# Performance work log

Measured on AMD Instinct MI355X. Metric: run time of the kernel, lower is better.

The kernel has to match this reference:

```python
import jax, jax.numpy as jnp
import numpy as np

NEG_SLOPE = 0.2  # PyG GATConv default leaky_relu slope
EPS = 1e-16     # PyG softmax denominator epsilon


def gat_conv(x, src, dst, W, att_src, att_dst, bias, concat, num_nodes):
    """PyG-style GATConv (eval mode, dropout disabled).
    x: [N, F_in]; W: [F_in, H*C]; att_src/att_dst: [H, C]; bias: [H*C] or [C].
    Messages flow src -> dst; softmax is per destination node."""
    H, C = att_src.shape
    h = (x @ W).reshape(num_nodes, H, C)                      # [N,H,C]
    a_src = jnp.sum(h * att_src[None], axis=-1)               # [N,H]
    a_dst = jnp.sum(h * att_dst[None], axis=-1)               # [N,H]
    e = jax.nn.leaky_relu(a_src[src] + a_dst[dst], NEG_SLOPE) # [E,H]
    # numerically-stable segment softmax over edges grouped by dst
    m = jax.ops.segment_max(e, dst, num_segments=num_nodes)   # [N,H]
    ex = jnp.exp(e - m[dst])                                  # [E,H]
    s = jax.ops.segment_sum(ex, dst, num_segments=num_nodes)  # [N,H]
    alpha = ex / (s[dst] + EPS)                               # [E,H]
    msg = h[src] * alpha[..., None]                           # [E,H,C]
    out = jax.ops.segment_sum(msg, dst, num_segments=num_nodes)  # [N,H,C]
    if concat:
        out = out.reshape(num_nodes, H * C)
    else:
        out = out.mean(axis=1)                                # [N,C]
    return out + bias, alpha


def setup_inputs() -> dict:
    key = jax.random.key(0)
    ks = jax.random.split(key, 20)
    N, E = 50000, 500000
    F_node = 128       # num_node_features
    SED = 128          # sentence_embedding_dim
    HID = 64           # hidden_channels
    H = 2              # num_heads

    def g(k, shape, scale=0.05):
        return jax.random.normal(k, shape, dtype=jnp.float32) * scale

    return {
        "x": jax.random.normal(ks[0], (N, SED), dtype=jnp.float32),
        "edge_index": jax.random.randint(ks[1], (2, E), 0, N, dtype=jnp.int64),
        "cls_emb": jax.random.normal(ks[2], (768,), dtype=jnp.float32),
        # fc0: Linear(768, SED)
        "fc0_w": g(ks[3], (SED, 768)), "fc0_b": g(ks[4], (SED,)),
        # conv1: GATConv(2*SED -> HID, heads=H, concat=True)
        "W1": g(ks[5], (2 * SED, H * HID)),
        "att_src1": g(ks[6], (H, HID)), "att_dst1": g(ks[7], (H, HID)),
        "bias1": g(ks[8], (H * HID,)),
        # conv2: GATConv(H*HID -> F_node, heads=H, concat=False)
        "W2": g(ks[9], (H * HID, H * F_node)),
        "att_src2": g(ks[10], (H, F_node)), "att_dst2": g(ks[11], (H, F_node)),
        "bias2": g(ks[12], (F_node,)),
        # edge MLP head
        "fc2_w": g(ks[13], (F_node, 2 * F_node)), "fc2_b": g(ks[14], (F_node,)),
        "fc3_w": g(ks[15], (1, F_node)), "fc3_b": g(ks[16], (1,)),
    }


def reference(x, edge_index, cls_emb, fc0_w, fc0_b,
              W1, att_src1, att_dst1, bias1,
              W2, att_src2, att_dst2, bias2,
              fc2_w, fc2_b, fc3_w, fc3_b):
    N = x.shape[0]
    src, dst = edge_index[0], edge_index[1]
    # sentence embedding projection + broadcast-concat to every node
    sent = fc0_w @ cls_emb + fc0_b                                # [SED]
    h = jnp.concatenate([x, jnp.broadcast_to(sent, (N, sent.shape[0]))], axis=1)
    h, _ = gat_conv(h, src, dst, W1, att_src1, att_dst1, bias1, True, N)
    h = jax.nn.elu(h)
    h, _ = gat_conv(h, src, dst, W2, att_src2, att_dst2, bias2, False, N)
    # edge head: gather endpoints, concat, MLP, sigmoid
    edge_input = jnp.concatenate([h[src], h[dst]], axis=1)        # [E, 2*F]
    z = jax.nn.relu(edge_input @ fc2_w.T + fc2_b)                 # [E, F]
    logits = z @ fc3_w.T + fc3_b                                  # [E, 1]
    return jax.nn.sigmoid(logits)
```

## Files before the change

kernel.cpp:

```cpp
#include <hip/hip_runtime.h>
#include <hip/hip_bf16.h>
#include <math.h>


typedef short short8 __attribute__((ext_vector_type(8)));
typedef float floatx4 __attribute__((ext_vector_type(4)));
typedef float v2f __attribute__((ext_vector_type(2)));
typedef unsigned uint2v __attribute__((ext_vector_type(2)));

__device__ __forceinline__ float wave_allreduce_sum(float v) {
    #pragma unroll
    for (int off = 1; off < 64; off <<= 1) v += __shfl_xor(v, off, 64);
    return v;
}
__device__ __forceinline__ v2f bfpair(unsigned v) {
    uint2v t; t.x = v << 16; t.y = v & 0xFFFF0000u;
    return __builtin_bit_cast(v2f, t);
}
__device__ __forceinline__ unsigned short bfbits(float f) {
    return __builtin_bit_cast(unsigned short, __float2bfloat16(f));
}
__device__ __forceinline__ unsigned packbf(float a, float b) {
    return ((unsigned)bfbits(b) << 16) | (unsigned)bfbits(a);
}
__device__ __forceinline__ float lrelu(float v) { return v > 0.f ? v : 0.2f * v; }

__global__ void prep_kernel(const float* __restrict__ cls, const float* __restrict__ fc0_w,
                            const float* __restrict__ fc0_b, const float* __restrict__ W1,
                            const float* __restrict__ W2, const float* __restrict__ fc2_w,
                            float* __restrict__ c1,
                            __hip_bfloat16* __restrict__ w1frag,
                            __hip_bfloat16* __restrict__ w2frag,
                            __hip_bfloat16* __restrict__ fc2frag) {
    int tid = threadIdx.x;
    if (blockIdx.x == 0) {
        __shared__ float s_sent[128];
        if (tid < 128) {
            float acc = fc0_b[tid];
            const float* row = fc0_w + (size_t)tid * 768;
            for (int k = 0; k < 768; ++k) acc += row[k] * cls[k];
            s_sent[tid] = acc;
        }
        __syncthreads();
        if (tid < 128) {
            float acc = 0.f;
            for (int k = 0; k < 128; ++k) acc += s_sent[k] * W1[(128 + k) * 128 + tid];
            c1[tid] = acc;
        }
    }
    int gstride = gridDim.x * blockDim.x;
    int g = blockIdx.x * blockDim.x + tid;
    for (int i = g; i < 16384; i += gstride) {
        int j = i & 7, l = (i >> 3) & 63, nt = (i >> 9) & 7, kt = (i >> 12) & 3;
        int k = kt * 32 + (l >> 4) * 8 + j;
        int n = nt * 16 + (l & 15);
        w1frag[i] = __float2bfloat16(W1[k * 128 + n]);
    }
    for (int i = g; i < 32768; i += gstride) {
        int j = i & 7, l = (i >> 3) & 63, nt = (i >> 9) & 15, kt = (i >> 13) & 3;
        int k = kt * 32 + (l >> 4) * 8 + j;
        int n = nt * 16 + (l & 15);
        w2frag[i] = __float2bfloat16(W2[k * 256 + n]);
    }
    for (int i = g; i < 32768; i += gstride) {
        int j = i & 7, l = (i >> 3) & 63, nt = (i >> 9) & 15, kt = (i >> 13) & 3;
        int k = kt * 32 + (l >> 4) * 8 + j;
        int n = nt * 16 + (l & 15);
        float v = (n < 128) ? fc2_w[n * 256 + k] : fc2_w[(n - 128) * 256 + 128 + k];
        fc2frag[i] = __float2bfloat16(v);
    }
}

__global__ void count_kernel(const int* __restrict__ dst, int* __restrict__ counts, int E) {
    int e = blockIdx.x * blockDim.x + threadIdx.x;
    if (e < E) atomicAdd(&counts[dst[e]], 1);
}

__global__ void __launch_bounds__(256) bsum_kernel(const int* __restrict__ counts,
                                                   int* __restrict__ bsum, int N) {
    int base = blockIdx.x * 1024;
    int tid = threadIdx.x;
    int v = 0;
    #pragma unroll
    for (int k = 0; k < 4; ++k) {
        int idx = base + k * 256 + tid;
        if (idx < N) v += counts[idx];
    }
    #pragma unroll
    for (int off = 1; off < 64; off <<= 1) v += __shfl_xor(v, off, 64);
    __shared__ int ws[4];
    if ((tid & 63) == 0) ws[tid >> 6] = v;
    __syncthreads();
    if (tid == 0) bsum[blockIdx.x] = ws[0] + ws[1] + ws[2] + ws[3];
}

__global__ void top_scan_kernel(const int* __restrict__ bsum, int* __restrict__ boff, int nb) {
    int lane = threadIdx.x;
    int v = (lane < nb) ? bsum[lane] : 0;
    int x = v;
    #pragma unroll
    for (int off = 1; off < 64; off <<= 1) {
        int t = __shfl_up(x, off, 64);
        if (lane >= off) x += t;
    }
    if (lane < nb) boff[lane] = x - v;
}

__global__ void __launch_bounds__(1024) local_scan_kernel(const int* __restrict__ counts,
                                                          const int* __restrict__ boff,
                                                          int* __restrict__ row, int* __restrict__ woff,
                                                          int N, int E) {
    int tid = threadIdx.x, lane = tid & 63, wv = tid >> 6;
    int base = blockIdx.x * 1024;
    __shared__ int wsum[16];
    int v = (base + tid < N) ? counts[base + tid] : 0;
    int x = v;
    #pragma unroll
    for (int off = 1; off < 64; off <<= 1) {
        int t = __shfl_up(x, off, 64);
        if (lane >= off) x += t;
    }
    if (lane == 63) wsum[wv] = x;
    __syncthreads();
    if (wv == 0 && lane < 16) {
        int y = wsum[lane];
        #pragma unroll
        for (int off = 1; off < 16; off <<= 1) {
            int t = __shfl_up(y, off, 64);
            if (lane >= off) y += t;
        }
        wsum[lane] = y;
    }
    __syncthreads();
    int excl = boff[blockIdx.x] + (wv ? wsum[wv - 1] : 0) + x - v;
    if (base + tid < N) { row[base + tid] = excl; woff[base + tid] = excl; }
    if (blockIdx.x == 0 && tid == 0) row[N] = E;
}

__global__ void scatter_kernel(const int* __restrict__ src, const int* __restrict__ dst,
                               int* __restrict__ woff, int* __restrict__ srcs, int E) {
    int e = blockIdx.x * blockDim.x + threadIdx.x;
    if (e < E) {
        int pos = atomicAdd(&woff[dst[e]], 1);
        srcs[pos] = src[e];
    }
}

__global__ void __launch_bounds__(256) gemm1_mfma_kernel(
        const float* __restrict__ x, const __hip_bfloat16* __restrict__ wfrag,
        const float* __restrict__ c1, const float* __restrict__ att_s, const float* __restrict__ att_d,
        __hip_bfloat16* __restrict__ h1bf, float* __restrict__ a_src, float* __restrict__ a_dst, int N) {
    int lane = threadIdx.x & 63, wv = threadIdx.x >> 6;
    int lo = lane & 15, quad = lane >> 4;
    int rowbase = (blockIdx.x * 4 + wv) * 16;
    if (rowbase >= N) return;
    int arow = rowbase + lo; if (arow >= N) arow = N - 1;
    const float* ap = x + (size_t)arow * 128 + quad * 8;
    floatx4 acc[8];
    #pragma unroll
    for (int nt = 0; nt < 8; ++nt) acc[nt] = (floatx4){0.f, 0.f, 0.f, 0.f};
    const short8* bf = (const short8*)wfrag;
    #pragma unroll
    for (int kt = 0; kt < 4; ++kt) {
        float4 fa = *(const float4*)(ap + kt * 32);
        float4 fb = *(const float4*)(ap + kt * 32 + 4);
        short8 a;
        a[0] = (short)bfbits(fa.x); a[1] = (short)bfbits(fa.y);
        a[2] = (short)bfbits(fa.z); a[3] = (short)bfbits(fa.w);
        a[4] = (short)bfbits(fb.x); a[5] = (short)bfbits(fb.y);
        a[6] = (short)bfbits(fb.z); a[7] = (short)bfbits(fb.w);
        #pragma unroll
        for (int nt = 0; nt < 8; ++nt)
            acc[nt] = __builtin_amdgcn_mfma_f32_16x16x32_bf16(a, bf[(kt * 8 + nt) * 64 + lane], acc[nt], 0, 0, 0);
    }
    float ps0[4] = {0,0,0,0}, ps1[4] = {0,0,0,0}, pd0[4] = {0,0,0,0}, pd1[4] = {0,0,0,0};
    #pragma unroll
    for (int nt = 0; nt < 8; ++nt) {
        int ch = nt * 16 + lo;
        float cv = c1[ch], as_v = att_s[ch], ad_v = att_d[ch];
        #pragma unroll
        for (int r = 0; r < 4; ++r) {
            int row = rowbase + quad * 4 + r;
            float val = acc[nt][r] + cv;
            if (row < N) ((unsigned short*)h1bf)[(size_t)row * 128 + ch] = bfbits(val);
            if (nt < 4) { ps0[r] += val * as_v; pd0[r] += val * ad_v; }
            else        { ps1[r] += val * as_v; pd1[r] += val * ad_v; }
        }
    }
    #pragma unroll
    for (int r = 0; r < 4; ++r) {
        int row = rowbase + quad * 4 + r;
        float v0 = ps0[r], v1 = ps1[r], v2 = pd0[r], v3 = pd1[r];
        #pragma unroll
        for (int off = 1; off < 16; off <<= 1) {
            v0 += __shfl_xor(v0, off, 64); v1 += __shfl_xor(v1, off, 64);
            v2 += __shfl_xor(v2, off, 64); v3 += __shfl_xor(v3, off, 64);
        }
        if (lo == 0 && row < N) {
            a_src[row * 2 + 0] = v0; a_src[row * 2 + 1] = v1;
            a_dst[row * 2 + 0] = v2; a_dst[row * 2 + 1] = v3;
        }
    }
}

__global__ void __launch_bounds__(256) agg1_csr_kernel(
        const int* __restrict__ row, const int* __restrict__ srcs,
        const float* __restrict__ a_src, const float* __restrict__ a_dst,
        const unsigned* __restrict__ h1u, const float* __restrict__ bias1,
        unsigned* __restrict__ hmid_u, int N) {
    int d = blockIdx.x * 4 + (threadIdx.x >> 6);
    if (d >= N) return;
    int lane = threadIdx.x & 63;
    int beg = row[d], end = row[d + 1];
    int g = lane >> 4, q = lane & 15;
    float2 adp = ((const float2*)a_dst)[d];
    float den0 = 0.f, den1 = 0.f;
    v2f facc2[4];
    #pragma unroll
    for (int m = 0; m < 4; ++m) facc2[m] = (v2f){0.f, 0.f};
    for (int b = beg; b < end; b += 64) {
        int i = b + lane;
        int s = 0; float e0 = 0.f, e1 = 0.f;
        if (i < end) {
            s = srcs[i];
            float2 as = ((const float2*)a_src)[s];
            e0 = __expf(lrelu(as.x + adp.x));
            e1 = __expf(lrelu(as.y + adp.y));
            den0 += e0; den1 += e1;
        }
        int cnt = min(64, end - b);
        int rounds = (cnt + 3) >> 2;
        float w0 = __shfl(e0, g, 64);
        float w1 = __shfl(e1, g, 64);
        int   sj = __shfl(s,  g, 64);
        float wgt = (q < 8) ? w0 : w1;
        uint4 u = ((const uint4*)(h1u + (size_t)sj * 64))[q];
        for (int j = 0; j < rounds; ++j) {
            int sl2 = 4 * j + 4 + g; sl2 = sl2 > 63 ? 63 : sl2;
            float w0n = __shfl(e0, sl2, 64);
            float w1n = __shfl(e1, sl2, 64);
            int   sjn = __shfl(s,  sl2, 64);
            uint4 un = ((const uint4*)(h1u + (size_t)sjn * 64))[q];
            float wgtn = (q < 8) ? w0n : w1n;
            facc2[0] += bfpair(u.x) * wgt;
            facc2[1] += bfpair(u.y) * wgt;
            facc2[2] += bfpair(u.z) * wgt;
            facc2[3] += bfpair(u.w) * wgt;
            u = un; wgt = wgtn;
        }
    }
    den0 = wave_allreduce_sum(den0);
    den1 = wave_allreduce_sum(den1);
    #pragma unroll
    for (int m = 0; m < 4; ++m) {
        facc2[m].x += __shfl_xor(facc2[m].x, 16, 64);
        facc2[m].y += __shfl_xor(facc2[m].y, 16, 64);
        facc2[m].x += __shfl_xor(facc2[m].x, 32, 64);
        facc2[m].y += __shfl_xor(facc2[m].y, 32, 64);
    }
    if (lane < 16) {
        float inv = (lane < 8) ? 1.f / (den0 + 1e-16f) : 1.f / (den1 + 1e-16f);
        int c0 = 8 * lane;
        float v[8];
        #pragma unroll
        for (int m = 0; m < 4; ++m) {
            float va = facc2[m].x * inv + bias1[c0 + 2 * m];
            float vb = facc2[m].y * inv + bias1[c0 + 2 * m + 1];
            v[2 * m]     = va > 0.f ? va : expm1f(va);
            v[2 * m + 1] = vb > 0.f ? vb : expm1f(vb);
        }
        uint4 o;
        o.x = packbf(v[0], v[1]); o.y = packbf(v[2], v[3]);
        o.z = packbf(v[4], v[5]); o.w = packbf(v[6], v[7]);
        ((uint4*)(hmid_u + (size_t)d * 64))[lane] = o;
    }
}

__global__ void __launch_bounds__(256) gemm2_mfma_kernel(
        const __hip_bfloat16* __restrict__ hmid, const __hip_bfloat16* __restrict__ wfrag,
        const float* __restrict__ att_s, const float* __restrict__ att_d,
        __hip_bfloat16* __restrict__ h2pre, float* __restrict__ a_src, float* __restrict__ a_dst, int N) {
    int lane = threadIdx.x & 63, wv = threadIdx.x >> 6;
    int lo = lane & 15, quad = lane >> 4;
    int rowbase = (blockIdx.x * 4 + wv) * 16;
    if (rowbase >= N) return;
    int arow = rowbase + lo; if (arow >= N) arow = N - 1;
    const __hip_bfloat16* ap = hmid + (size_t)arow * 128 + quad * 8;
    floatx4 acc[16];
    #pragma unroll
    for (int nt = 0; nt < 16; ++nt) acc[nt] = (floatx4){0.f, 0.f, 0.f, 0.f};
    const short8* bf = (const short8*)wfrag;
    #pragma unroll
    for (int kt = 0; kt < 4; ++kt) {
        short8 a = *(const short8*)(ap + kt * 32);
        #pragma unroll
        for (int nt = 0; nt < 16; ++nt)
            acc[nt] = __builtin_amdgcn_mfma_f32_16x16x32_bf16(a, bf[(kt * 16 + nt) * 64 + lane], acc[nt], 0, 0, 0);
    }
    float ps0[4] = {0,0,0,0}, ps1[4] = {0,0,0,0}, pd0[4] = {0,0,0,0}, pd1[4] = {0,0,0,0};
    #pragma unroll
    for (int nt = 0; nt < 16; ++nt) {
        int ch = nt * 16 + lo;
        float as_v = att_s[ch], ad_v = att_d[ch];
        #pragma unroll
        for (int r = 0; r < 4; ++r) {
            int row = rowbase + quad * 4 + r;
            float val = acc[nt][r];
            if (row < N) ((unsigned short*)h2pre)[(size_t)row * 256 + ch] = bfbits(val);
            if (nt < 8) { ps0[r] += val * as_v; pd0[r] += val * ad_v; }
            else        { ps1[r] += val * as_v; pd1[r] += val * ad_v; }
        }
    }
    #pragma unroll
    for (int r = 0; r < 4; ++r) {
        int row = rowbase + quad * 4 + r;
        float v0 = ps0[r], v1 = ps1[r], v2 = pd0[r], v3 = pd1[r];
        #pragma unroll
        for (int off = 1; off < 16; off <<= 1) {
            v0 += __shfl_xor(v0, off, 64); v1 += __shfl_xor(v1, off, 64);
            v2 += __shfl_xor(v2, off, 64); v3 += __shfl_xor(v3, off, 64);
        }
        if (lo == 0 && row < N) {
            a_src[row * 2 + 0] = v0; a_src[row * 2 + 1] = v1;
            a_dst[row * 2 + 0] = v2; a_dst[row * 2 + 1] = v3;
        }
    }
}

__global__ void __launch_bounds__(256) agg2_csr_kernel(
        const int* __restrict__ row, const int* __restrict__ srcs,
        const float* __restrict__ a_src, const float* __restrict__ a_dst,
        const unsigned* __restrict__ h2u, const float* __restrict__ bias2,
        unsigned* __restrict__ h2bf_u, int N) {
    int d = blockIdx.x * 4 + (threadIdx.x >> 6);
    if (d >= N) return;
    int lane = threadIdx.x & 63;
    int beg = row[d], end = row[d + 1];
    int g = lane >> 5, q = lane & 31;
    float2 adp = ((const float2*)a_dst)[d];
    float den0 = 0.f, den1 = 0.f;
    v2f facc2[4];
    #pragma unroll
    for (int m = 0; m < 4; ++m) facc2[m] = (v2f){0.f, 0.f};
    for (int b = beg; b < end; b += 64) {
        int i = b + lane;
        int s = 0; float e0 = 0.f, e1 = 0.f;
        if (i < end) {
            s = srcs[i];
            float2 as = ((const float2*)a_src)[s];
            e0 = __expf(lrelu(as.x + adp.x));
            e1 = __expf(lrelu(as.y + adp.y));
            den0 += e0; den1 += e1;
        }
        int cnt = min(64, end - b);
        int rounds = (cnt + 1) >> 1;
        float w0 = __shfl(e0, g, 64);
        float w1 = __shfl(e1, g, 64);
        int   sj = __shfl(s,  g, 64);
        float wgt = (q < 16) ? w0 : w1;
        uint4 u = ((const uint4*)(h2u + (size_t)sj * 128))[q];
        for (int j = 0; j < rounds; ++j) {
            int sl2 = 2 * j + 2 + g; sl2 = sl2 > 63 ? 63 : sl2;
            float w0n = __shfl(e0, sl2, 64);
            float w1n = __shfl(e1, sl2, 64);
            int   sjn = __shfl(s,  sl2, 64);
            uint4 un = ((const uint4*)(h2u + (size_t)sjn * 128))[q];
            float wgtn = (q < 16) ? w0n : w1n;
            facc2[0] += bfpair(u.x) * wgt;
            facc2[1] += bfpair(u.y) * wgt;
            facc2[2] += bfpair(u.z) * wgt;
            facc2[3] += bfpair(u.w) * wgt;
            u = un; wgt = wgtn;
        }
    }
    den0 = wave_allreduce_sum(den0);
    den1 = wave_allreduce_sum(den1);
    float inv = (q < 16) ? 0.5f / (den0 + 1e-16f) : 0.5f / (den1 + 1e-16f);
    #pragma unroll
    for (int m = 0; m < 4; ++m) {
        facc2[m].x += __shfl_xor(facc2[m].x, 32, 64);
        facc2[m].y += __shfl_xor(facc2[m].y, 32, 64);
        facc2[m] *= inv;
        facc2[m].x += __shfl_xor(facc2[m].x, 16, 64);
        facc2[m].y += __shfl_xor(facc2[m].y, 16, 64);
    }
    if (lane < 16) {
        int c0 = 8 * lane;
        uint4 o;
        o.x = packbf(facc2[0].x + bias2[c0 + 0], facc2[0].y + bias2[c0 + 1]);
        o.y = packbf(facc2[1].x + bias2[c0 + 2], facc2[1].y + bias2[c0 + 3]);
        o.z = packbf(facc2[2].x + bias2[c0 + 4], facc2[2].y + bias2[c0 + 5]);
        o.w = packbf(facc2[3].x + bias2[c0 + 6], facc2[3].y + bias2[c0 + 7]);
        ((uint4*)(h2bf_u + (size_t)d * 64))[lane] = o;
    }
}

__global__ void __launch_bounds__(256) zsd_mfma_kernel(
        const __hip_bfloat16* __restrict__ h2bf, const __hip_bfloat16* __restrict__ wfrag,
        const float* __restrict__ fc2_b, __hip_bfloat16* __restrict__ zsd, int N) {
    int lane = threadIdx.x & 63, wv = threadIdx.x >> 6;
    int lo = lane & 15, quad = lane >> 4;
    int rowbase = (blockIdx.x * 4 + wv) * 16;
    if (rowbase >= N) return;
    int arow = rowbase + lo; if (arow >= N) arow = N - 1;
    const __hip_bfloat16* ap = h2bf + (size_t)arow * 128 + quad * 8;
    floatx4 acc[16];
    #pragma unroll
    for (int nt = 0; nt < 16; ++nt) acc[nt] = (floatx4){0.f, 0.f, 0.f, 0.f};
    const short8* bf = (const short8*)wfrag;
    #pragma unroll
    for (int kt = 0; kt < 4; ++kt) {
        short8 a = *(const short8*)(ap + kt * 32);
        #pragma unroll
        for (int nt = 0; nt < 16; ++nt)
            acc[nt] = __builtin_amdgcn_mfma_f32_16x16x32_bf16(a, bf[(kt * 16 + nt) * 64 + lane], acc[nt], 0, 0, 0);
    }
    #pragma unroll
    for (int nt = 0; nt < 16; ++nt) {
        int ch = nt * 16 + lo;
        float bv = (nt >= 8) ? fc2_b[ch - 128] : 0.f;
        #pragma unroll
        for (int r = 0; r < 4; ++r) {
            int row = rowbase + quad * 4 + r;
            if (row < N) ((unsigned short*)zsd)[(size_t)row * 256 + ch] = bfbits(acc[nt][r] + bv);
        }
    }
}

__global__ void __launch_bounds__(256) edge_zsd_kernel(
        const int* __restrict__ src, const int* __restrict__ dst,
        const unsigned* __restrict__ zsd_u, const float* __restrict__ fc3_w,
        const float* __restrict__ fc3_b, float* __restrict__ out, int E) {
    int lane = threadIdx.x & 63, wv = threadIdx.x >> 6;
    int g = lane >> 5, r = (lane >> 4) & 1, q = lane & 15;
    int base = (blockIdx.x * 4 + wv) * 16;
    if (base >= E) return;
    v2f f30 = {fc3_w[8 * q + 4 * r + 0], fc3_w[8 * q + 4 * r + 1]};
    v2f f31 = {fc3_w[8 * q + 4 * r + 2], fc3_w[8 * q + 4 * r + 3]};
    float b3 = fc3_b[0];
    #pragma unroll
    for (int j = 0; j < 8; ++j) {
        int e = base + 2 * j + g;
        int ec = e < E ? e : E - 1;
        int node = r ? dst[ec] : src[ec];
        uint4 mine = ((const uint4*)(zsd_u + (size_t)node * 128 + (r << 6)))[q];
        unsigned sx = (unsigned)__shfl_xor((int)mine.x, 16, 64);
        unsigned sy = (unsigned)__shfl_xor((int)mine.y, 16, 64);
        unsigned sz = (unsigned)__shfl_xor((int)mine.z, 16, 64);
        unsigned sw = (unsigned)__shfl_xor((int)mine.w, 16, 64);
        unsigned mA = r ? mine.z : mine.x;
        unsigned mB = r ? mine.w : mine.y;
        unsigned oA = r ? sz : sx;
        unsigned oB = r ? sw : sy;
        v2f sA = bfpair(mA) + bfpair(oA);
        v2f sB = bfpair(mB) + bfpair(oB);
        sA.x = fmaxf(sA.x, 0.f); sA.y = fmaxf(sA.y, 0.f);
        sB.x = fmaxf(sB.x, 0.f); sB.y = fmaxf(sB.y, 0.f);
        v2f p2 = sA * f30 + sB * f31;
        float p = p2.x + p2.y;
        #pragma unroll
        for (int off = 1; off < 32; off <<= 1) p += __shfl_xor(p, off, 64);
        if ((lane & 31) == 0 && e < E)
            out[e] = 1.f / (1.f + expf(-(p + b3)));
    }
}

extern "C" void kernel_launch(void* const* d_in, const int* in_sizes, int n_in,
                              void* d_out, int out_size, void* d_ws, size_t ws_size,
                              hipStream_t stream) {
    const float* x      = (const float*)d_in[0];
    const int*   ei     = (const int*)d_in[1];
    const float* cls    = (const float*)d_in[2];
    const float* fc0_w  = (const float*)d_in[3];
    const float* fc0_b  = (const float*)d_in[4];
    const float* W1     = (const float*)d_in[5];
    const float* att_s1 = (const float*)d_in[6];
    const float* att_d1 = (const float*)d_in[7];
    const float* bias1  = (const float*)d_in[8];
    const float* W2     = (const float*)d_in[9];
    const float* att_s2 = (const float*)d_in[10];
    const float* att_d2 = (const float*)d_in[11];
    const float* bias2  = (const float*)d_in[12];
    const float* fc2_w  = (const float*)d_in[13];
    const float* fc2_b  = (const float*)d_in[14];
    const float* fc3_w  = (const float*)d_in[15];
    const float* fc3_b  = (const float*)d_in[16];
    float* out = (float*)d_out;

    int N = in_sizes[0] / 128;
    int E = in_sizes[1] / 2;
    const int* src = ei;
    const int* dst = ei + E;
    int nb = (N + 1023) / 1024;

    float* w = (float*)d_ws;
    size_t off = 0;
    auto alloc = [&](size_t n) { float* p = w + off; off += (n + 63) & ~(size_t)63; return p; };
    float* c1      = alloc(128);
    float* w1fragf = alloc(16384 / 2);
    float* w2fragf = alloc(32768 / 2);
    float* fc2fragf= alloc(32768 / 2);
    float* a_s1    = alloc((size_t)N * 2);
    float* a_d1    = alloc((size_t)N * 2);
    float* a_s2    = alloc((size_t)N * 2);
    float* a_d2    = alloc((size_t)N * 2);
    float* h1bff   = alloc((size_t)N * 64);
    float* hmidf   = alloc((size_t)N * 64);
    float* h2pref  = alloc((size_t)N * 128);
    float* h2bff   = alloc((size_t)N * 64);
    float* zsdf    = alloc((size_t)N * 128);
    int* counts = (int*)alloc(N);
    int* rowp   = (int*)alloc(N + 1);
    int* woff   = (int*)alloc(N);
    int* srcs   = (int*)alloc(E);
    int* bsum   = (int*)alloc(64);
    int* boff   = (int*)alloc(64);
    __hip_bfloat16* w1frag = (__hip_bfloat16*)w1fragf;
    __hip_bfloat16* w2frag = (__hip_bfloat16*)w2fragf;
    __hip_bfloat16* fc2frag= (__hip_bfloat16*)fc2fragf;
    __hip_bfloat16* hmid   = (__hip_bfloat16*)hmidf;
    __hip_bfloat16* h2pre  = (__hip_bfloat16*)h2pref;
    __hip_bfloat16* h2bf   = (__hip_bfloat16*)h2bff;
    __hip_bfloat16* h1bf   = (__hip_bfloat16*)h1bff;
    __hip_bfloat16* zsd    = (__hip_bfloat16*)zsdf;

    hipMemsetAsync(counts, 0, sizeof(int) * (size_t)N, stream);

    prep_kernel<<<64, 256, 0, stream>>>(cls, fc0_w, fc0_b, W1, W2, fc2_w, c1, w1frag, w2frag, fc2frag);
    count_kernel<<<(E + 255) / 256, 256, 0, stream>>>(dst, counts, E);
    bsum_kernel<<<nb, 256, 0, stream>>>(counts, bsum, N);
    top_scan_kernel<<<1, 64, 0, stream>>>(bsum, boff, nb);
    local_scan_kernel<<<nb, 1024, 0, stream>>>(counts, boff, rowp, woff, N, E);
    scatter_kernel<<<(E + 255) / 256, 256, 0, stream>>>(src, dst, woff, srcs, E);
    gemm1_mfma_kernel<<<(N + 63) / 64, 256, 0, stream>>>(x, w1frag, c1, att_s1, att_d1, h1bf, a_s1, a_d1, N);
    agg1_csr_kernel<<<(N + 3) / 4, 256, 0, stream>>>(rowp, srcs, a_s1, a_d1, (const unsigned*)h1bf, bias1, (unsigned*)hmid, N);
    gemm2_mfma_kernel<<<(N + 63) / 64, 256, 0, stream>>>(hmid, w2frag, att_s2, att_d2, h2pre, a_s2, a_d2, N);
    agg2_csr_kernel<<<(N + 3) / 4, 256, 0, stream>>>(rowp, srcs, a_s2, a_d2, (const unsigned*)h2pre, bias2, (unsigned*)h2bf, N);
    zsd_mfma_kernel<<<(N + 63) / 64, 256, 0, stream>>>(h2bf, fc2frag, fc2_b, zsd, N);
    edge_zsd_kernel<<<(E + 63) / 64, 256, 0, stream>>>(src, dst, (const unsigned*)zsd, fc3_w, fc3_b, out, E);
}
```

Baseline: 361.0 us.

## Map aggregation to sub-wave groups per node, fuse count into gemm1, batch edge loads

```diff
diff --git a/kernel.cpp b/kernel.cpp
--- a/kernel.cpp
+++ b/kernel.cpp
@@ -8,11 +8,6 @@
 typedef float v2f __attribute__((ext_vector_type(2)));
 typedef unsigned uint2v __attribute__((ext_vector_type(2)));
 
-__device__ __forceinline__ float wave_allreduce_sum(float v) {
-    #pragma unroll
-    for (int off = 1; off < 64; off <<= 1) v += __shfl_xor(v, off, 64);
-    return v;
-}
 __device__ __forceinline__ v2f bfpair(unsigned v) {
     uint2v t; t.x = v << 16; t.y = v & 0xFFFF0000u;
     return __builtin_bit_cast(v2f, t);
@@ -71,11 +66,6 @@
     }
 }
 
-__global__ void count_kernel(const int* __restrict__ dst, int* __restrict__ counts, int E) {
-    int e = blockIdx.x * blockDim.x + threadIdx.x;
-    if (e < E) atomicAdd(&counts[dst[e]], 1);
-}
-
 __global__ void __launch_bounds__(256) bsum_kernel(const int* __restrict__ counts,
                                                    int* __restrict__ bsum, int N) {
     int base = blockIdx.x * 1024;
@@ -146,13 +136,19 @@
     }
 }
 
-__global__ void __launch_bounds__(256) gemm1_mfma_kernel(
+__global__ void __launch_bounds__(256) gemm1_count_kernel(
         const float* __restrict__ x, const __hip_bfloat16* __restrict__ wfrag,
         const float* __restrict__ c1, const float* __restrict__ att_s, const float* __restrict__ att_d,
-        __hip_bfloat16* __restrict__ h1bf, float* __restrict__ a_src, float* __restrict__ a_dst, int N) {
+        __hip_bfloat16* __restrict__ h1bf, float* __restrict__ a_src, float* __restrict__ a_dst,
+        const int* __restrict__ dst, int* __restrict__ counts, int E, int G1, int N) {
+    if ((int)blockIdx.x >= G1) {
+        int e = ((int)blockIdx.x - G1) * 256 + threadIdx.x;
+        if (e < E) atomicAdd(&counts[dst[e]], 1);
+        return;
+    }
     int lane = threadIdx.x & 63, wv = threadIdx.x >> 6;
     int lo = lane & 15, quad = lane >> 4;
-    int rowbase = (blockIdx.x * 4 + wv) * 16;
+    int rowbase = ((int)blockIdx.x * 4 + wv) * 16;
     if (rowbase >= N) return;
     int arow = rowbase + lo; if (arow >= N) arow = N - 1;
     const float* ap = x + (size_t)arow * 128 + quad * 8;
@@ -208,72 +204,51 @@
         const float* __restrict__ a_src, const float* __restrict__ a_dst,
         const unsigned* __restrict__ h1u, const float* __restrict__ bias1,
         unsigned* __restrict__ hmid_u, int N) {
-    int d = blockIdx.x * 4 + (threadIdx.x >> 6);
+    int tid = threadIdx.x;
+    int d = blockIdx.x * 16 + (tid >> 4);
     if (d >= N) return;
-    int lane = threadIdx.x & 63;
+    int q = tid & 15;
     int beg = row[d], end = row[d + 1];
-    int g = lane >> 4, q = lane & 15;
     float2 adp = ((const float2*)a_dst)[d];
     float den0 = 0.f, den1 = 0.f;
     v2f facc2[4];
     #pragma unroll
     for (int m = 0; m < 4; ++m) facc2[m] = (v2f){0.f, 0.f};
-    for (int b = beg; b < end; b += 64) {
-        int i = b + lane;
-        int s = 0; float e0 = 0.f, e1 = 0.f;
-        if (i < end) {
-            s = srcs[i];
-            float2 as = ((const float2*)a_src)[s];
-            e0 = __expf(lrelu(as.x + adp.x));
-            e1 = __expf(lrelu(as.y + adp.y));
-            den0 += e0; den1 += e1;
-        }
-        int cnt = min(64, end - b);
-        int rounds = (cnt + 3) >> 2;
-        float w0 = __shfl(e0, g, 64);
-        float w1 = __shfl(e1, g, 64);
-        int   sj = __shfl(s,  g, 64);
-        float wgt = (q < 8) ? w0 : w1;
-        uint4 u = ((const uint4*)(h1u + (size_t)sj * 64))[q];
-        for (int j = 0; j < rounds; ++j) {
-            int sl2 = 4 * j + 4 + g; sl2 = sl2 > 63 ? 63 : sl2;
-            float w0n = __shfl(e0, sl2, 64);
-            float w1n = __shfl(e1, sl2, 64);
-            int   sjn = __shfl(s,  sl2, 64);
-            uint4 un = ((const uint4*)(h1u + (size_t)sjn * 64))[q];
-            float wgtn = (q < 8) ? w0n : w1n;
-            facc2[0] += bfpair(u.x) * wgt;
-            facc2[1] += bfpair(u.y) * wgt;
-            facc2[2] += bfpair(u.z) * wgt;
-            facc2[3] += bfpair(u.w) * wgt;
-            u = un; wgt = wgtn;
-        }
-    }
-    den0 = wave_allreduce_sum(den0);
-    den1 = wave_allreduce_sum(den1);
+    for (int i = beg; i < end; i += 2) {
+        int s0 = srcs[i];
+        bool has1 = (i + 1) < end;
+        int s1 = has1 ? srcs[i + 1] : s0;
+        float2 as0 = ((const float2*)a_src)[s0];
+        float2 as1 = ((const float2*)a_src)[s1];
+        uint4 u0 = ((const uint4*)(h1u + (size_t)s0 * 64))[q];
+        uint4 u1 = ((const uint4*)(h1u + (size_t)s1 * 64))[q];
+        float e00 = __expf(lrelu(as0.x + adp.x));
+        float e01 = __expf(lrelu(as0.y + adp.y));
+        float e10 = has1 ? __expf(lrelu(as1.x + adp.x)) : 0.f;
+        float e11 = has1 ? __expf(lrelu(as1.y + adp.y)) : 0.f;
+        den0 += e00 + e10;
+        den1 += e01 + e11;
+        float w0 = (q < 8) ? e00 : e01;
+        float w1 = (q < 8) ? e10 : e11;
+        facc2[0] += bfpair(u0.x) * w0 + bfpair(u1.x) * w1;
+        facc2[1] += bfpair(u0.y) * w0 + bfpair(u1.y) * w1;
+        facc2[2] += bfpair(u0.z) * w0 + bfpair(u1.z) * w1;
+        facc2[3] += bfpair(u0.w) * w0 + bfpair(u1.w) * w1;
+    }
+    float inv = 1.f / (((q < 8) ? den0 : den1) + 1e-16f);
+    int c0 = 8 * q;
+    float v[8];
     #pragma unroll
     for (int m = 0; m < 4; ++m) {
-        facc2[m].x += __shfl_xor(facc2[m].x, 16, 64);
-        facc2[m].y += __shfl_xor(facc2[m].y, 16, 64);
-        facc2[m].x += __shfl_xor(facc2[m].x, 32, 64);
-        facc2[m].y += __shfl_xor(facc2[m].y, 32, 64);
-    }
-    if (lane < 16) {
-        float inv = (lane < 8) ? 1.f / (den0 + 1e-16f) : 1.f / (den1 + 1e-16f);
-        int c0 = 8 * lane;
-        float v[8];
-        #pragma unroll
-        for (int m = 0; m < 4; ++m) {
-            float va = facc2[m].x * inv + bias1[c0 + 2 * m];
-            float vb = facc2[m].y * inv + bias1[c0 + 2 * m + 1];
-            v[2 * m]     = va > 0.f ? va : expm1f(va);
-            v[2 * m + 1] = vb > 0.f ? vb : expm1f(vb);
-        }
-        uint4 o;
-        o.x = packbf(v[0], v[1]); o.y = packbf(v[2], v[3]);
-        o.z = packbf(v[4], v[5]); o.w = packbf(v[6], v[7]);
-        ((uint4*)(hmid_u + (size_t)d * 64))[lane] = o;
-    }
+        float va = facc2[m].x * inv + bias1[c0 + 2 * m];
+        float vb = facc2[m].y * inv + bias1[c0 + 2 * m + 1];
+        v[2 * m]     = va > 0.f ? va : expm1f(va);
+        v[2 * m + 1] = vb > 0.f ? vb : expm1f(vb);
+    }
+    uint4 o;
+    o.x = packbf(v[0], v[1]); o.y = packbf(v[2], v[3]);
+    o.z = packbf(v[4], v[5]); o.w = packbf(v[6], v[7]);
+    ((uint4*)(hmid_u + (size_t)d * 64))[q] = o;
 }
 
 __global__ void __launch_bounds__(256) gemm2_mfma_kernel(
@@ -332,66 +307,52 @@
         const float* __restrict__ a_src, const float* __restrict__ a_dst,
         const unsigned* __restrict__ h2u, const float* __restrict__ bias2,
         unsigned* __restrict__ h2bf_u, int N) {
-    int d = blockIdx.x * 4 + (threadIdx.x >> 6);
+    int tid = threadIdx.x;
+    int d = blockIdx.x * 8 + (tid >> 5);
     if (d >= N) return;
-    int lane = threadIdx.x & 63;
+    int q = tid & 31;
     int beg = row[d], end = row[d + 1];
-    int g = lane >> 5, q = lane & 31;
     float2 adp = ((const float2*)a_dst)[d];
     float den0 = 0.f, den1 = 0.f;
     v2f facc2[4];
     #pragma unroll
     for (int m = 0; m < 4; ++m) facc2[m] = (v2f){0.f, 0.f};
-    for (int b = beg; b < end; b += 64) {
-        int i = b + lane;
-        int s = 0; float e0 = 0.f, e1 = 0.f;
-        if (i < end) {
-            s = srcs[i];
-            float2 as = ((const float2*)a_src)[s];
-            e0 = __expf(lrelu(as.x + adp.x));
-            e1 = __expf(lrelu(as.y + adp.y));
-            den0 += e0; den1 += e1;
-        }
-        int cnt = min(64, end - b);
-        int rounds = (cnt + 1) >> 1;
-        float w0 = __shfl(e0, g, 64);
-        float w1 = __shfl(e1, g, 64);
-        int   sj = __shfl(s,  g, 64);
-        float wgt = (q < 16) ? w0 : w1;
-        uint4 u = ((const uint4*)(h2u + (size_t)sj * 128))[q];
-        for (int j = 0; j < rounds; ++j) {
-            int sl2 = 2 * j + 2 + g; sl2 = sl2 > 63 ? 63 : sl2;
-            float w0n = __shfl(e0, sl2, 64);
-            float w1n = __shfl(e1, sl2, 64);
-            int   sjn = __shfl(s,  sl2, 64);
-            uint4 un = ((const uint4*)(h2u + (size_t)sjn * 128))[q];
-            float wgtn = (q < 16) ? w0n : w1n;
-            facc2[0] += bfpair(u.x) * wgt;
-            facc2[1] += bfpair(u.y) * wgt;
-            facc2[2] += bfpair(u.z) * wgt;
-            facc2[3] += bfpair(u.w) * wgt;
-            u = un; wgt = wgtn;
-        }
-    }
-    den0 = wave_allreduce_sum(den0);
-    den1 = wave_allreduce_sum(den1);
-    float inv = (q < 16) ? 0.5f / (den0 + 1e-16f) : 0.5f / (den1 + 1e-16f);
+    for (int i = beg; i < end; i += 2) {
+        int s0 = srcs[i];
+        bool has1 = (i + 1) < end;
+        int s1 = has1 ? srcs[i + 1] : s0;
+        float2 as0 = ((const float2*)a_src)[s0];
+        float2 as1 = ((const float2*)a_src)[s1];
+        uint4 u0 = ((const uint4*)(h2u + (size_t)s0 * 128))[q];
+        uint4 u1 = ((const uint4*)(h2u + (size_t)s1 * 128))[q];
+        float e00 = __expf(lrelu(as0.x + adp.x));
+        float e01 = __expf(lrelu(as0.y + adp.y));
+        float e10 = has1 ? __expf(lrelu(as1.x + adp.x)) : 0.f;
+        float e11 = has1 ? __expf(lrelu(as1.y + adp.y)) : 0.f;
+        den0 += e00 + e10;
+        den1 += e01 + e11;
+        float w0 = (q < 16) ? e00 : e01;
+        float w1 = (q < 16) ? e10 : e11;
+        facc2[0] += bfpair(u0.x) * w0 + bfpair(u1.x) * w1;
+        facc2[1] += bfpair(u0.y) * w0 + bfpair(u1.y) * w1;
+        facc2[2] += bfpair(u0.z) * w0 + bfpair(u1.z) * w1;
+        facc2[3] += bfpair(u0.w) * w0 + bfpair(u1.w) * w1;
+    }
+    float inv = 0.5f / (((q < 16) ? den0 : den1) + 1e-16f);
     #pragma unroll
     for (int m = 0; m < 4; ++m) {
-        facc2[m].x += __shfl_xor(facc2[m].x, 32, 64);
-        facc2[m].y += __shfl_xor(facc2[m].y, 32, 64);
         facc2[m] *= inv;
         facc2[m].x += __shfl_xor(facc2[m].x, 16, 64);
         facc2[m].y += __shfl_xor(facc2[m].y, 16, 64);
     }
-    if (lane < 16) {
-        int c0 = 8 * lane;
+    if (q < 16) {
+        int c0 = 8 * q;
         uint4 o;
         o.x = packbf(facc2[0].x + bias2[c0 + 0], facc2[0].y + bias2[c0 + 1]);
         o.y = packbf(facc2[1].x + bias2[c0 + 2], facc2[1].y + bias2[c0 + 3]);
         o.z = packbf(facc2[2].x + bias2[c0 + 4], facc2[2].y + bias2[c0 + 5]);
         o.w = packbf(facc2[3].x + bias2[c0 + 6], facc2[3].y + bias2[c0 + 7]);
-        ((uint4*)(h2bf_u + (size_t)d * 64))[lane] = o;
+        ((uint4*)(h2bf_u + (size_t)d * 64))[q] = o;
     }
 }
 
@@ -438,12 +399,20 @@
     v2f f30 = {fc3_w[8 * q + 4 * r + 0], fc3_w[8 * q + 4 * r + 1]};
     v2f f31 = {fc3_w[8 * q + 4 * r + 2], fc3_w[8 * q + 4 * r + 3]};
     float b3 = fc3_b[0];
+    int nodes[8];
     #pragma unroll
     for (int j = 0; j < 8; ++j) {
         int e = base + 2 * j + g;
         int ec = e < E ? e : E - 1;
-        int node = r ? dst[ec] : src[ec];
-        uint4 mine = ((const uint4*)(zsd_u + (size_t)node * 128 + (r << 6)))[q];
+        nodes[j] = r ? dst[ec] : src[ec];
+    }
+    uint4 rows[8];
+    #pragma unroll
+    for (int j = 0; j < 8; ++j)
+        rows[j] = ((const uint4*)(zsd_u + (size_t)nodes[j] * 128 + (r << 6)))[q];
+    #pragma unroll
+    for (int j = 0; j < 8; ++j) {
+        uint4 mine = rows[j];
         unsigned sx = (unsigned)__shfl_xor((int)mine.x, 16, 64);
         unsigned sy = (unsigned)__shfl_xor((int)mine.y, 16, 64);
         unsigned sz = (unsigned)__shfl_xor((int)mine.z, 16, 64);
@@ -460,6 +429,7 @@
         float p = p2.x + p2.y;
         #pragma unroll
         for (int off = 1; off < 32; off <<= 1) p += __shfl_xor(p, off, 64);
+        int e = base + 2 * j + g;
         if ((lane & 31) == 0 && e < E)
             out[e] = 1.f / (1.f + expf(-(p + b3)));
     }
@@ -527,15 +497,17 @@
     hipMemsetAsync(counts, 0, sizeof(int) * (size_t)N, stream);
 
     prep_kernel<<<64, 256, 0, stream>>>(cls, fc0_w, fc0_b, W1, W2, fc2_w, c1, w1frag, w2frag, fc2frag);
-    count_kernel<<<(E + 255) / 256, 256, 0, stream>>>(dst, counts, E);
+    int G1 = (N + 63) / 64;
+    int G2 = (E + 255) / 256;
+    gemm1_count_kernel<<<G1 + G2, 256, 0, stream>>>(x, w1frag, c1, att_s1, att_d1, h1bf, a_s1, a_d1,
+                                                    dst, counts, E, G1, N);
     bsum_kernel<<<nb, 256, 0, stream>>>(counts, bsum, N);
     top_scan_kernel<<<1, 64, 0, stream>>>(bsum, boff, nb);
     local_scan_kernel<<<nb, 1024, 0, stream>>>(counts, boff, rowp, woff, N, E);
     scatter_kernel<<<(E + 255) / 256, 256, 0, stream>>>(src, dst, woff, srcs, E);
-    gemm1_mfma_kernel<<<(N + 63) / 64, 256, 0, stream>>>(x, w1frag, c1, att_s1, att_d1, h1bf, a_s1, a_d1, N);
-    agg1_csr_kernel<<<(N + 3) / 4, 256, 0, stream>>>(rowp, srcs, a_s1, a_d1, (const unsigned*)h1bf, bias1, (unsigned*)hmid, N);
+    agg1_csr_kernel<<<(N + 15) / 16, 256, 0, stream>>>(rowp, srcs, a_s1, a_d1, (const unsigned*)h1bf, bias1, (unsigned*)hmid, N);
     gemm2_mfma_kernel<<<(N + 63) / 64, 256, 0, stream>>>(hmid, w2frag, att_s2, att_d2, h2pre, a_s2, a_d2, N);
-    agg2_csr_kernel<<<(N + 3) / 4, 256, 0, stream>>>(rowp, srcs, a_s2, a_d2, (const unsigned*)h2pre, bias2, (unsigned*)h2bf, N);
+    agg2_csr_kernel<<<(N + 7) / 8, 256, 0, stream>>>(rowp, srcs, a_s2, a_d2, (const unsigned*)h2pre, bias2, (unsigned*)h2bf, N);
     zsd_mfma_kernel<<<(N + 63) / 64, 256, 0, stream>>>(h2bf, fc2frag, fc2_b, zsd, N);
     edge_zsd_kernel<<<(E + 63) / 64, 256, 0, stream>>>(src, dst, (const unsigned*)zsd, fc3_w, fc3_b, out, E);
 }
```

After: 336.3 us. 1.07x faster.
